# Performance work log

Measured on AMD Instinct MI355X. Metric: run time of the kernel, lower is better.

The kernel has to match this reference:

```python
import jax, jax.numpy as jnp
import numpy as np

HIDDEN = 2048
HEADS = 16
HEAD_DIM = HIDDEN // HEADS  # 128
ROPE_THETA = 10000.0


def rope_tables(L, d, theta, dtype=jnp.float32):
    inv_freq = 1.0 / (theta ** (jnp.arange(0, d, 2, dtype=jnp.float32) / d))  # [d/2]
    pos = jnp.arange(L, dtype=jnp.float32)
    freqs = pos[:, None] * inv_freq[None, :]            # [L, d/2]
    emb = jnp.concatenate([freqs, freqs], axis=-1)      # [L, d]
    return jnp.cos(emb).astype(dtype), jnp.sin(emb).astype(dtype)


def rotate_half(x):
    x1, x2 = jnp.split(x, 2, axis=-1)
    return jnp.concatenate([-x2, x1], axis=-1)


def setup_inputs() -> dict:
    key = jax.random.key(0)
    k1, k2, k3, k4, k5 = jax.random.split(key, 5)
    N, L = 2, 2048
    scale = 1.0 / np.sqrt(HIDDEN)
    return {
        "x": jax.random.normal(k1, (N, L, HIDDEN), dtype=jnp.float32),
        "wq": jax.random.normal(k2, (HIDDEN, HIDDEN), dtype=jnp.float32) * scale,
        "wk": jax.random.normal(k3, (HIDDEN, HIDDEN), dtype=jnp.float32) * scale,
        "wv": jax.random.normal(k4, (HIDDEN, HIDDEN), dtype=jnp.float32) * scale,
        "wo": jax.random.normal(k5, (HIDDEN, HIDDEN), dtype=jnp.float32) * scale,
    }


def reference(x, wq, wk, wv, wo):
    N, L, D = x.shape
    # QKV projections (torch Linear: y = x @ W.T)
    q = (x @ wq.T).reshape(N, L, HEADS, HEAD_DIM)
    k = (x @ wk.T).reshape(N, L, HEADS, HEAD_DIM)
    v = (x @ wv.T).reshape(N, L, HEADS, HEAD_DIM)
    # RoPE, broadcast over head dim (unsqueeze_dim=2)
    cos, sin = rope_tables(L, HEAD_DIM, ROPE_THETA, x.dtype)
    cos = cos[None, :, None, :]  # [1, L, 1, d]
    sin = sin[None, :, None, :]
    q = q * cos + rotate_half(q) * sin
    k = k * cos + rotate_half(k) * sin
    # causal SDPA over [N, H, L, d]
    scores = jnp.einsum("blhd,bmhd->bhlm", q, k) / jnp.sqrt(jnp.asarray(HEAD_DIM, x.dtype))
    causal = jnp.tril(jnp.ones((L, L), dtype=bool))
    scores = jnp.where(causal[None, None], scores, jnp.asarray(-jnp.inf, x.dtype))
    attn = jax.nn.softmax(scores, axis=-1)
    o = jnp.einsum("bhlm,bmhd->blhd", attn, v).reshape(N, L, D)
    return o @ wo.T
```

## Files before the change

### kernel.cpp

```cpp
#include <hip/hip_runtime.h>
#include <math.h>


typedef __bf16 bf16x8 __attribute__((ext_vector_type(8)));
typedef __bf16 bf16x4 __attribute__((ext_vector_type(4)));
typedef float  f32x4  __attribute__((ext_vector_type(4)));

#define AS1 __attribute__((address_space(1)))
#define AS3 __attribute__((address_space(3)))

static __device__ __forceinline__ void async_copy16(const void* g, void* l) {
  __builtin_amdgcn_global_load_lds((AS1 void*)g, (AS3 void*)l, 16, 0, 0);
}

__global__ __launch_bounds__(256) void cvt_all(
    const float* __restrict__ x,  const float* __restrict__ wq,
    const float* __restrict__ wk, const float* __restrict__ wv,
    const float* __restrict__ wo,
    __bf16* __restrict__ xb,  __bf16* __restrict__ wqb,
    __bf16* __restrict__ wkb, __bf16* __restrict__ wvb,
    __bf16* __restrict__ wob) {
  int i = blockIdx.x * 256 + threadIdx.x;
  const float* in; __bf16* out; int off;
  if (i < 2097152)      { in = x;  out = xb;  off = i; }
  else if (i < 3145728) { in = wq; out = wqb; off = i - 2097152; }
  else if (i < 4194304) { in = wk; out = wkb; off = i - 3145728; }
  else if (i < 5242880) { in = wv; out = wvb; off = i - 4194304; }
  else                  { in = wo; out = wob; off = i - 5242880; }
  float4 v = ((const float4*)in)[off];
  bf16x4 o;
  o[0] = (__bf16)v.x; o[1] = (__bf16)v.y; o[2] = (__bf16)v.z; o[3] = (__bf16)v.w;
  ((bf16x4*)out)[off] = o;
}

static __device__ __forceinline__ void gemm_core(const __bf16* __restrict__ A,
                                                 const __bf16* __restrict__ B,
                                                 int bm, int bn, f32x4 acc[4][4]) {
  constexpr int Kd = 2048;
  __shared__ __bf16 As[128 * 32];
  __shared__ __bf16 Bs[128 * 32];
  const int tid  = threadIdx.x;
  const int lane = tid & 63;
  const int wave = tid >> 6;
  const int l15 = lane & 15, l4 = lane >> 4;
  const int wm = (wave >> 1) * 64;
  const int cw = (wave & 1) * 32;

  const __bf16* Ag = A + (size_t)(bm + (tid >> 2)) * Kd + (tid & 3) * 8;
  const __bf16* Bg = B + (size_t)(bn + (tid >> 2)) * Kd + (tid & 3) * 8;
  __bf16* Asw = As + wave * 512;
  __bf16* Bsw = Bs + wave * 512;

  for (int k0 = 0; k0 < Kd; k0 += 32) {
    async_copy16(Ag + k0, Asw);
    async_copy16(Ag + (size_t)64 * Kd + k0, Asw + 2048);
    async_copy16(Bg + k0, Bsw);
    async_copy16(Bg + (size_t)64 * Kd + k0, Bsw + 2048);
    __syncthreads();
    bf16x8 af[4], bfr[4];
#pragma unroll
    for (int i = 0; i < 4; ++i)
      af[i] = *(const bf16x8*)&As[(wm + 16 * i + l15) * 32 + 8 * l4];
#pragma unroll
    for (int j = 0; j < 4; ++j)
      bfr[j] = *(const bf16x8*)&Bs[(cw + (j & 1) * 16 + (j >> 1) * 64 + l15) * 32 + 8 * l4];
#pragma unroll
    for (int i = 0; i < 4; ++i)
#pragma unroll
      for (int j = 0; j < 4; ++j)
        acc[i][j] = __builtin_amdgcn_mfma_f32_16x16x32_bf16(af[i], bfr[j], acc[i][j], 0, 0, 0);
    __syncthreads();
  }
}

__global__ __launch_bounds__(256) void gemm_qkv(const __bf16* __restrict__ A,
                                                const __bf16* __restrict__ wqb,
                                                const __bf16* __restrict__ wkb,
                                                const __bf16* __restrict__ wvb,
                                                __bf16* __restrict__ Qb,
                                                __bf16* __restrict__ Kb,
                                                __bf16* __restrict__ Vt) {
  const int z = blockIdx.z;
  const __bf16* B = (z == 0) ? wqb : (z == 1) ? wkb : wvb;
  const int bm = blockIdx.x * 128, bn = blockIdx.y * 128;
  f32x4 acc[4][4] = {};
  gemm_core(A, B, bm, bn, acc);

  const int lane = threadIdx.x & 63;
  const int wave = threadIdx.x >> 6;
  const int l15 = lane & 15, l4 = lane >> 4;
  const int wm = (wave >> 1) * 64;
  const int cw = (wave & 1) * 32;

  if (z < 2) {
    __bf16* C = z ? Kb : Qb;
    const float scale = z ? 1.0f : 0.08838834764831845f;
    float fr[2];
#pragma unroll
    for (int jp = 0; jp < 2; ++jp) {
      const int d = cw + jp * 16 + l15;
      fr[jp] = exp2f((float)d * -0.20762050593045f);
    }
#pragma unroll
    for (int i = 0; i < 4; ++i) {
      const int grow0 = bm + wm + 16 * i + 4 * l4;
#pragma unroll
      for (int jp = 0; jp < 2; ++jp) {
        const int gcol = bn + cw + jp * 16 + l15;
#pragma unroll
        for (int r = 0; r < 4; ++r) {
          const int pos = (grow0 + r) & 2047;
          const float th = (float)pos * fr[jp];
          const float cv = __cosf(th), sv = __sinf(th);
          const float a1 = acc[i][jp][r], a2 = acc[i][jp + 2][r];
          C[(size_t)(grow0 + r) * 2048 + gcol]      = (__bf16)((a1 * cv - a2 * sv) * scale);
          C[(size_t)(grow0 + r) * 2048 + gcol + 64] = (__bf16)((a2 * cv + a1 * sv) * scale);
        }
      }
    }
  } else {
#pragma unroll
    for (int i = 0; i < 4; ++i) {
      const int grow0 = bm + wm + 16 * i + 4 * l4;
      const int bb = grow0 >> 11, ll = grow0 & 2047;
#pragma unroll
      for (int j = 0; j < 4; ++j) {
        const int gcol = bn + cw + (j & 1) * 16 + (j >> 1) * 64 + l15;
        bf16x4 pk;
#pragma unroll
        for (int r = 0; r < 4; ++r) pk[r] = (__bf16)acc[i][j][r];
        *(bf16x4*)(Vt + ((size_t)(bb * 2048 + gcol)) * 2048 + ll) = pk;
      }
    }
  }
}

__global__ __launch_bounds__(256) void gemm_out(const __bf16* __restrict__ A,
                                                const __bf16* __restrict__ B,
                                                float* __restrict__ C) {
  const int bm = blockIdx.x * 128, bn = blockIdx.y * 128;
  f32x4 acc[4][4] = {};
  gemm_core(A, B, bm, bn, acc);
  const int lane = threadIdx.x & 63;
  const int wave = threadIdx.x >> 6;
  const int l15 = lane & 15, l4 = lane >> 4;
  const int wm = (wave >> 1) * 64;
  const int cw = (wave & 1) * 32;
#pragma unroll
  for (int i = 0; i < 4; ++i) {
    const int grow0 = bm + wm + 16 * i + 4 * l4;
#pragma unroll
    for (int j = 0; j < 4; ++j) {
      const int gcol = bn + cw + (j & 1) * 16 + (j >> 1) * 64 + l15;
#pragma unroll
      for (int r = 0; r < 4; ++r)
        C[(size_t)(grow0 + r) * 2048 + gcol] = acc[i][j][r];
    }
  }
}

__global__ __launch_bounds__(256) void attn_flash(const __bf16* __restrict__ Q,
                                                  const __bf16* __restrict__ Km,
                                                  const __bf16* __restrict__ Vt,
                                                  __bf16* __restrict__ O) {
  __shared__ __bf16 Ks[2][4096];
  __shared__ __bf16 Vs[2][4096];
  __shared__ __bf16 Pl[4][1024];
  const int lane = threadIdx.x & 63;
  const int wave = threadIdx.x >> 6;
  const int l15 = lane & 15, l4 = lane >> 4;

  const int id = blockIdx.x;
  const int xcd = id & 7, jj = id >> 3;
  const int g = jj >> 4;
  const int bh = xcd + 8 * g;
  const int qb = ((jj & 15) + 4 * g) & 15;
  const int qbase = qb * 128;
  const int b = bh >> 4, h = bh & 15;
  const int qw0 = qbase + wave * 32;

  const int srow = lane >> 2, sc = lane & 3;
  const __bf16* Kg0 = Km + ((size_t)(b * 2048 + srow)) * 2048 + h * 128 + wave * 32 + sc * 8;
  const __bf16* Vg0 = Vt + ((size_t)(b * 2048 + h * 128 + wave * 32 + srow)) * 2048 + sc * 8;

  bf16x8 aq[2][4];
#pragma unroll
  for (int m = 0; m < 2; ++m) {
    const __bf16* Qb2 = Q + ((size_t)(b * 2048 + qw0 + 16 * m + l15)) * 2048 + h * 128 + 8 * l4;
#pragma unroll
    for (int st = 0; st < 4; ++st) aq[m][st] = *(const bf16x8*)(Qb2 + st * 32);
  }

  bf16x8 ones;
#pragma unroll
  for (int q = 0; q < 8; ++q) ones[q] = (__bf16)1.0f;

  f32x4 oa[2][8] = {};
  f32x4 os[2] = {};

  const int nkb = qb * 4 + 4;

  async_copy16(Kg0,                     &Ks[0][wave * 1024]);
  async_copy16(Kg0 + (size_t)16 * 2048, &Ks[0][wave * 1024 + 512]);
  async_copy16(Vg0,                     &Vs[0][wave * 1024]);
  async_copy16(Vg0 + (size_t)16 * 2048, &Vs[0][wave * 1024 + 512]);

  for (int kb = 0; kb < nkb; ++kb) {
    const int buf = kb & 1;
    __syncthreads();
    if (kb + 1 < nkb) {
      const size_t koff = (size_t)(kb + 1) * 32 * 2048;
      const int nb = buf ^ 1;
      async_copy16(Kg0 + koff,                      &Ks[nb][wave * 1024]);
      async_copy16(Kg0 + koff + (size_t)16 * 2048,  &Ks[nb][wave * 1024 + 512]);
      async_copy16(Vg0 + (kb + 1) * 32,             &Vs[nb][wave * 1024]);
      async_copy16(Vg0 + (kb + 1) * 32 + (size_t)16 * 2048, &Vs[nb][wave * 1024 + 512]);
    }
    const int kpos = kb * 32;

    f32x4 s[2][2] = {};
#pragma unroll
    for (int nt = 0; nt < 2; ++nt)
#pragma unroll
      for (int st = 0; st < 4; ++st) {
        bf16x8 bk = *(const bf16x8*)&Ks[buf][st * 1024 + (nt * 16 + l15) * 32 + 8 * l4];
#pragma unroll
        for (int m = 0; m < 2; ++m)
          s[m][nt] = __builtin_amdgcn_mfma_f32_16x16x32_bf16(aq[m][st], bk, s[m][nt], 0, 0, 0);
      }

#pragma unroll
    for (int m = 0; m < 2; ++m) {
      const int qwm = qw0 + 16 * m;
      const bool diag = (kpos + 31 > qwm);
      __bf16* pw = &Pl[wave][m * 512];
#pragma unroll
      for (int nt = 0; nt < 2; ++nt) {
        const int col = kpos + nt * 16 + l15;
#pragma unroll
        for (int r = 0; r < 4; ++r) {
          float p = __expf(fminf(s[m][nt][r], 40.f));
          if (diag && col > qwm + 4 * l4 + r) p = 0.f;
          pw[(4 * l4 + r) * 32 + nt * 16 + l15] = (__bf16)p;
        }
      }
    }
    bf16x8 ap[2];
#pragma unroll
    for (int m = 0; m < 2; ++m) {
      ap[m] = *(const bf16x8*)&Pl[wave][m * 512 + l15 * 32 + 8 * l4];
      os[m] = __builtin_amdgcn_mfma_f32_16x16x32_bf16(ap[m], ones, os[m], 0, 0, 0);
    }
#pragma unroll
    for (int dt = 0; dt < 8; ++dt) {
      bf16x8 bv = *(const bf16x8*)&Vs[buf][dt * 512 + l15 * 32 + 8 * l4];
#pragma unroll
      for (int m = 0; m < 2; ++m)
        oa[m][dt] = __builtin_amdgcn_mfma_f32_16x16x32_bf16(ap[m], bv, oa[m][dt], 0, 0, 0);
    }
  }

#pragma unroll
  for (int m = 0; m < 2; ++m) {
    float inv[4];
#pragma unroll
    for (int r = 0; r < 4; ++r) inv[r] = 1.0f / os[m][r];
    __bf16* Obase = O + ((size_t)(b * 2048 + qw0 + 16 * m + 4 * l4)) * 2048 + h * 128;
#pragma unroll
    for (int dt = 0; dt < 8; ++dt)
#pragma unroll
      for (int r = 0; r < 4; ++r)
        Obase[(size_t)r * 2048 + dt * 16 + l15] = (__bf16)(oa[m][dt][r] * inv[r]);
  }
}

extern "C" void kernel_launch(void* const* d_in, const int* in_sizes, int n_in,
                              void* d_out, int out_size, void* d_ws, size_t ws_size,
                              hipStream_t stream) {
  const float* x  = (const float*)d_in[0];
  const float* wq = (const float*)d_in[1];
  const float* wk = (const float*)d_in[2];
  const float* wv = (const float*)d_in[3];
  const float* wo = (const float*)d_in[4];

  char* ws = (char*)d_ws;
  __bf16* xb  = (__bf16*)(ws + 0);
  __bf16* wqb = (__bf16*)(ws + 16777216);
  __bf16* wkb = (__bf16*)(ws + 25165824);
  __bf16* wvb = (__bf16*)(ws + 33554432);
  __bf16* wob = (__bf16*)(ws + 41943040);
  __bf16* Qb  = (__bf16*)(ws + 50331648);
  __bf16* Kb  = (__bf16*)(ws + 67108864);
  __bf16* Vt  = (__bf16*)(ws + 83886080);
  __bf16* Ob  = xb;

  cvt_all<<<24576, 256, 0, stream>>>(x, wq, wk, wv, wo, xb, wqb, wkb, wvb, wob);

  gemm_qkv<<<dim3(32, 16, 3), 256, 0, stream>>>(xb, wqb, wkb, wvb, Qb, Kb, Vt);

  attn_flash<<<512, 256, 0, stream>>>(Qb, Kb, Vt, Ob);

  gemm_out<<<dim3(32, 16), 256, 0, stream>>>(Ob, wob, (float*)d_out);
}
```

Baseline: 389.3 us.

## Widen attention key block to 64 and read V directly from global memory

The flash attention kernel now processes 64 keys per iteration instead of 32, halving the loop trip count and the number of barriers. K is still staged in LDS with double buffering, while V tiles are loaded straight from global memory into registers for the PV MFMAs, dropping the V LDS staging. The P scratch buffer in LDS uses an XOR swizzle to reduce bank conflicts. The exchange is more register pressure and uncached-latency global V loads that are not prefetched, which may stall the MFMA chain.

```diff
diff --git a/kernel.cpp b/kernel.cpp
--- a/kernel.cpp
+++ b/kernel.cpp
@@ -163,9 +163,8 @@
                                                   const __bf16* __restrict__ Km,
                                                   const __bf16* __restrict__ Vt,
                                                   __bf16* __restrict__ O) {
-  __shared__ __bf16 Ks[2][4096];
-  __shared__ __bf16 Vs[2][4096];
-  __shared__ __bf16 Pl[4][1024];
+  __shared__ __bf16 Ks[2][8192];
+  __shared__ __bf16 Pl[4][2048];
   const int lane = threadIdx.x & 63;
   const int wave = threadIdx.x >> 6;
   const int l15 = lane & 15, l4 = lane >> 4;
@@ -179,9 +178,10 @@
   const int b = bh >> 4, h = bh & 15;
   const int qw0 = qbase + wave * 32;
 
-  const int srow = lane >> 2, sc = lane & 3;
-  const __bf16* Kg0 = Km + ((size_t)(b * 2048 + srow)) * 2048 + h * 128 + wave * 32 + sc * 8;
-  const __bf16* Vg0 = Vt + ((size_t)(b * 2048 + h * 128 + wave * 32 + srow)) * 2048 + sc * 8;
+  const __bf16* Kg0 = Km + ((size_t)(b * 2048 + wave * 16 + (lane >> 2))) * 2048
+                         + h * 128 + (lane & 3) * 8;
+
+  const __bf16* Vg0 = Vt + ((size_t)(b * 2048 + h * 128 + l15)) * 2048 + 8 * l4;
 
   bf16x8 aq[2][4];
 #pragma unroll
@@ -198,32 +198,30 @@
   f32x4 oa[2][8] = {};
   f32x4 os[2] = {};
 
-  const int nkb = qb * 4 + 4;
-
-  async_copy16(Kg0,                     &Ks[0][wave * 1024]);
-  async_copy16(Kg0 + (size_t)16 * 2048, &Ks[0][wave * 1024 + 512]);
-  async_copy16(Vg0,                     &Vs[0][wave * 1024]);
-  async_copy16(Vg0 + (size_t)16 * 2048, &Vs[0][wave * 1024 + 512]);
+  const int nkb = qb * 2 + 2;
+
+#pragma unroll
+  for (int st = 0; st < 4; ++st)
+    async_copy16(Kg0 + st * 32, &Ks[0][st * 2048 + wave * 512]);
 
   for (int kb = 0; kb < nkb; ++kb) {
     const int buf = kb & 1;
     __syncthreads();
     if (kb + 1 < nkb) {
-      const size_t koff = (size_t)(kb + 1) * 32 * 2048;
+      const size_t koff = (size_t)(kb + 1) * 64 * 2048;
       const int nb = buf ^ 1;
-      async_copy16(Kg0 + koff,                      &Ks[nb][wave * 1024]);
-      async_copy16(Kg0 + koff + (size_t)16 * 2048,  &Ks[nb][wave * 1024 + 512]);
-      async_copy16(Vg0 + (kb + 1) * 32,             &Vs[nb][wave * 1024]);
-      async_copy16(Vg0 + (kb + 1) * 32 + (size_t)16 * 2048, &Vs[nb][wave * 1024 + 512]);
-    }
-    const int kpos = kb * 32;
-
-    f32x4 s[2][2] = {};
-#pragma unroll
-    for (int nt = 0; nt < 2; ++nt)
-#pragma unroll
-      for (int st = 0; st < 4; ++st) {
-        bf16x8 bk = *(const bf16x8*)&Ks[buf][st * 1024 + (nt * 16 + l15) * 32 + 8 * l4];
+#pragma unroll
+      for (int st = 0; st < 4; ++st)
+        async_copy16(Kg0 + koff + st * 32, &Ks[nb][st * 2048 + wave * 512]);
+    }
+    const int kpos = kb * 64;
+
+    f32x4 s[2][4] = {};
+#pragma unroll
+    for (int st = 0; st < 4; ++st)
+#pragma unroll
+      for (int nt = 0; nt < 4; ++nt) {
+        bf16x8 bk = *(const bf16x8*)&Ks[buf][st * 2048 + (nt * 16 + l15) * 32 + 8 * l4];
 #pragma unroll
         for (int m = 0; m < 2; ++m)
           s[m][nt] = __builtin_amdgcn_mfma_f32_16x16x32_bf16(aq[m][st], bk, s[m][nt], 0, 0, 0);
@@ -232,32 +230,45 @@
 #pragma unroll
     for (int m = 0; m < 2; ++m) {
       const int qwm = qw0 + 16 * m;
-      const bool diag = (kpos + 31 > qwm);
-      __bf16* pw = &Pl[wave][m * 512];
-#pragma unroll
-      for (int nt = 0; nt < 2; ++nt) {
+      const bool diag = (kpos + 63 > qwm);
+      __bf16* pw = &Pl[wave][m * 1024];
+#pragma unroll
+      for (int nt = 0; nt < 4; ++nt) {
         const int col = kpos + nt * 16 + l15;
+        const int cin = nt * 2 + (l15 >> 3);
 #pragma unroll
         for (int r = 0; r < 4; ++r) {
           float p = __expf(fminf(s[m][nt][r], 40.f));
           if (diag && col > qwm + 4 * l4 + r) p = 0.f;
-          pw[(4 * l4 + r) * 32 + nt * 16 + l15] = (__bf16)p;
+          const int rw = 4 * l4 + r;
+          pw[rw * 64 + ((cin ^ (rw & 7)) * 8) + (l15 & 7)] = (__bf16)p;
         }
       }
     }
-    bf16x8 ap[2];
-#pragma unroll
-    for (int m = 0; m < 2; ++m) {
-      ap[m] = *(const bf16x8*)&Pl[wave][m * 512 + l15 * 32 + 8 * l4];
-      os[m] = __builtin_amdgcn_mfma_f32_16x16x32_bf16(ap[m], ones, os[m], 0, 0, 0);
-    }
-#pragma unroll
-    for (int dt = 0; dt < 8; ++dt) {
-      bf16x8 bv = *(const bf16x8*)&Vs[buf][dt * 512 + l15 * 32 + 8 * l4];
-#pragma unroll
-      for (int m = 0; m < 2; ++m)
-        oa[m][dt] = __builtin_amdgcn_mfma_f32_16x16x32_bf16(ap[m], bv, oa[m][dt], 0, 0, 0);
-    }
+
+    bf16x8 ap[2][2];
+#pragma unroll
+    for (int m = 0; m < 2; ++m)
+#pragma unroll
+      for (int ks = 0; ks < 2; ++ks)
+        ap[m][ks] = *(const bf16x8*)&Pl[wave][m * 1024 + l15 * 64 + ((ks * 4 + l4) ^ (l15 & 7)) * 8];
+
+#pragma unroll
+    for (int m = 0; m < 2; ++m)
+#pragma unroll
+      for (int ks = 0; ks < 2; ++ks)
+        os[m] = __builtin_amdgcn_mfma_f32_16x16x32_bf16(ap[m][ks], ones, os[m], 0, 0, 0);
+
+    const __bf16* Vg = Vg0 + kpos;
+#pragma unroll
+    for (int dt = 0; dt < 8; ++dt)
+#pragma unroll
+      for (int ks = 0; ks < 2; ++ks) {
+        bf16x8 bv = *(const bf16x8*)(Vg + (size_t)dt * 16 * 2048 + ks * 32);
+#pragma unroll
+        for (int m = 0; m < 2; ++m)
+          oa[m][dt] = __builtin_amdgcn_mfma_f32_16x16x32_bf16(ap[m][ks], bv, oa[m][dt], 0, 0, 0);
+      }
   }
 
 #pragma unroll
```

New measurement: 461.6 us. 1.19x slower.
